# Optimization experiments

Hardware: AMD Instinct MI355X
Metric: run time of the kernel (lower is better)

Reference implementation:

```python
import jax, jax.numpy as jnp
import numpy as np

N_CONST = 1.0
M_CONST = 11008.0

def setup_inputs() -> dict:
    key = jax.random.key(0)
    ks = jax.random.split(key, 7)
    N, LM_D, GNN_D, H = 131072, 1024, 200, 128
    lm_embeds = jax.random.normal(ks[0], (N, LM_D), dtype=jnp.float32)
    gnn_embeds = jax.random.normal(ks[1], (N, GNN_D), dtype=jnp.float32)
    neg_gnn_embeds = jax.random.normal(ks[2], (N, GNN_D), dtype=jnp.float32)
    lm_W = jax.random.normal(ks[3], (LM_D, H), dtype=jnp.float32) * (1.0 / np.sqrt(LM_D))
    lm_b = jnp.zeros((H,), dtype=jnp.float32)
    gnn_W = jax.random.normal(ks[4], (GNN_D, H), dtype=jnp.float32) * (1.0 / np.sqrt(GNN_D))
    gnn_b = jnp.zeros((H,), dtype=jnp.float32)
    return {"lm_embeds": lm_embeds, "gnn_embeds": gnn_embeds,
            "neg_gnn_embeds": neg_gnn_embeds,
            "lm_W": lm_W, "lm_b": lm_b, "gnn_W": gnn_W, "gnn_b": gnn_b}

def _l2norm(x):
    return x / jnp.linalg.norm(x, axis=-1, keepdims=True)

def _cal(lm_in, gnn_in, lm_W, lm_b, gnn_W, gnn_b, neg):
    l = _l2norm(lm_in @ lm_W + lm_b)       # [N, H]
    g = _l2norm(gnn_in @ gnn_W + gnn_b)    # [N, H]
    # diagonal of l @ g.T == per-row dot product (avoids NxN matmul)
    logits = jnp.exp(jnp.sum(l * g, axis=-1))  # [N]
    ratio = logits / (logits + N_CONST / M_CONST)
    return jnp.log(1.0 - ratio) if neg else jnp.log(ratio)

def reference(lm_embeds, gnn_embeds, neg_gnn_embeds, lm_W, lm_b, gnn_W, gnn_b):
    pos = jnp.mean(_cal(lm_embeds, gnn_embeds, lm_W, lm_b, gnn_W, gnn_b, False))
    neg = jnp.mean(_cal(lm_embeds, neg_gnn_embeds, lm_W, lm_b, gnn_W, gnn_b, True))
    return -pos - neg
```

## Files before the change

kernel.cpp:

```cpp
#include <hip/hip_runtime.h>
#include <hip/hip_bf16.h>
#include <stdint.h>

#define NROWS 131072
#define LMD   1024
#define GNND  200
#define HD    128
#define BLOCK 256
#define MTILE 64
#define NBLK  (NROWS/MTILE)
#define WCH   16384

typedef __attribute__((ext_vector_type(4))) float  f32x4;
typedef __attribute__((ext_vector_type(8))) short  bf16x8;

#define GLDS(SRC, DST) __builtin_amdgcn_global_load_lds( \
    (const __attribute__((address_space(1))) unsigned int*)(SRC), \
    (__attribute__((address_space(3))) unsigned int*)(DST), 16, 0, 0)
#define SCHED0  __builtin_amdgcn_sched_barrier(0)
#define BAR     __builtin_amdgcn_s_barrier()
#define VMW(N)  asm volatile("s_waitcnt vmcnt(" #N ")" ::: "memory")

__device__ __forceinline__ short f2bf(float x) {
    union { __hip_bfloat16 h; short s; } u;
    u.h = __float2bfloat16(x);
    return u.s;
}

__device__ __forceinline__ bf16x8 cvt8(f32x4 a, f32x4 b) {
    bf16x8 r;
    r[0]=f2bf(a[0]); r[1]=f2bf(a[1]); r[2]=f2bf(a[2]); r[3]=f2bf(a[3]);
    r[4]=f2bf(b[0]); r[5]=f2bf(b[1]); r[6]=f2bf(b[2]); r[7]=f2bf(b[3]);
    return r;
}

__device__ __forceinline__ float red16(float v) {
    #pragma unroll
    for (int m=1; m<16; m<<=1) v += __shfl_xor(v, m, 16);
    return v;
}

__global__ void prep_weights(const float* __restrict__ lm_W,
                             const float* __restrict__ gnn_W,
                             short* __restrict__ W1S, short* __restrict__ W2S)
{
    int idx = blockIdx.x*BLOCK + threadIdx.x;
    int row = (idx >> 6) & 127;
    int e   = idx & 63;
    int kk  = (idx >> 13)*64 + (e ^ ((row & 7)*8));
    W1S[idx] = f2bf(lm_W[(long)kk*HD + row]);
    if (idx < 4*8192) {
        W2S[idx] = (kk < GNND) ? f2bf(gnn_W[(long)kk*HD + row]) : (short)0;
    }
}

__global__ __launch_bounds__(BLOCK) void fused(
    const float* __restrict__ lm,  const float* __restrict__ gnn,
    const float* __restrict__ ngn,
    const float* __restrict__ lm_b, const float* __restrict__ gnn_b,
    const char* __restrict__ W1S,  const char* __restrict__ W2S,
    float* __restrict__ partials)
{
    __shared__ short lbuf[4*8192];
    __shared__ float sp[4], sn[4];

    const int tid  = threadIdx.x;
    const int lane = tid & 63;
    const int win  = tid >> 6;
    const int col  = lane & 15;
    const int g    = lane >> 4;
    const int wq   = win*4096 + lane*16;
    const long row = (long)blockIdx.x * MTILE + win*16 + col;

    const char* aL = (const char*)lm  + row*(LMD*4L)  + g*32;
    const char* aG = (const char*)gnn + row*(GNND*4L) + g*32;
    const char* aN = (const char*)ngn + row*(GNND*4L) + g*32;
    const char* clampG = (const char*)gnn + (size_t)NROWS*GNND*4 - 16;
    const char* clampN = (const char*)ngn + (size_t)NROWS*GNND*4 - 16;

    const float CC   = 1.0f / 11008.0f;
    const float LOGC = -9.3063777f;
    const f32x4 fz = {0.f,0.f,0.f,0.f};

    auto ISSUEW = [&](int x) {
        const char* ws = (x < 16 ? W1S + (size_t)x*WCH : W2S + (size_t)(x-16)*WCH) + wq;
        char* wd = (char*)lbuf + (size_t)(x & 3)*WCH + wq;
        #pragma unroll
        for (int i=0;i<4;i++) GLDS(ws + i*1024, wd + i*1024);
    };
    auto LOADG = [&](const char* base, int off, const char* cl, f32x4 (&S)[8]) {
        #pragma unroll
        for (int j=0;j<4;j++) {
            const char* p0 = base + off + j*128;
            const char* p1 = p0 + 16;
            if (cl) { if (p0 > cl) p0 = cl;  if (p1 > cl) p1 = cl; }
            S[2*j]   = *(const f32x4*)p0;
            S[2*j+1] = *(const f32x4*)p1;
        }
    };
    auto COMP = [&](int c, int half, f32x4 (&S)[8], f32x4 (&acc)[8]) {
        const short* wb = lbuf + (c & 3)*8192 + col*64;
        const int sw = (col & 7)*8;
        #pragma unroll
        for (int ks=0; ks<2; ++ks) {
            bf16x8 af = cvt8(S[half*4 + 2*ks], S[half*4 + 2*ks + 1]);
            const short* cb = wb + ((ks*32 + g*8) ^ sw);
            #pragma unroll
            for (int t=0;t<8;t++) {
                bf16x8 wf = *(const bf16x8*)(cb + t*1024);
                acc[t] = __builtin_amdgcn_mfma_f32_16x16x32_bf16(af, wf, acc[t], 0,0,0);
            }
        }
    };

    f32x4 accL[8], accG[8];
    #pragma unroll
    for (int t=0;t<8;t++) accL[t] = fz;
    f32x4 SA[8], SB[8];
    float pos_acc = 0.f, neg_acc = 0.f;

    float bl[8], bg[8];
    #pragma unroll
    for (int t=0;t<8;t++) bl[t] = lm_b[t*16+col];
    #pragma unroll
    for (int t=0;t<8;t++) bg[t] = gnn_b[t*16+col];
    SCHED0;
    ISSUEW(0); ISSUEW(1); ISSUEW(2);
    LOADG(aL,   0, nullptr, SA);
    LOADG(aL, 512, nullptr, SB);
    SCHED0; VMW(24); SCHED0; BAR; SCHED0;
    #pragma unroll
    for (int t=0;t<8;t++) { asm volatile("" : "+v"(bl[t])); asm volatile("" : "+v"(bg[t])); }

    #pragma unroll
    for (int gg=0; gg<8; ++gg) {
        f32x4 (&S)[8] = (gg & 1) ? SB : SA;
        ISSUEW(2*gg+3);
        SCHED0;
        COMP(2*gg, 0, S, accL);
        SCHED0; VMW(16); SCHED0; BAR; SCHED0;
        ISSUEW(2*gg+4);
        SCHED0;
        COMP(2*gg+1, 1, S, accL);
        SCHED0;
        if (gg < 6)       LOADG(aL, (gg+2)*512, nullptr, S);
        else if (gg == 6) LOADG(aG,   0, clampG, S);
        else              LOADG(aG, 512, clampG, S);
        SCHED0; VMW(24); SCHED0; BAR; SCHED0;
    }

    #pragma unroll
    for (int t=0;t<8;t++) {
        #pragma unroll
        for (int r=0;r<4;r++) accL[t][r] += bl[t];
    }
    #pragma unroll
    for (int t=0;t<8;t++) accG[t] = fz;

    ISSUEW(19);
    SCHED0;
    COMP(16, 0, SA, accG);
    SCHED0; VMW(16); SCHED0; BAR; SCHED0;

    COMP(17, 1, SA, accG);
    SCHED0;
    LOADG(aN, 0, clampN, SA);
    SCHED0; VMW(20); SCHED0; BAR; SCHED0;

    COMP(18, 0, SB, accG);
    SCHED0; VMW(8); SCHED0; BAR; SCHED0;

    COMP(19, 1, SB, accG);
    SCHED0;
    LOADG(aN, 512, clampN, SB);
    SCHED0;

    #pragma unroll
    for (int r=0;r<4;r++) {
        float lg=0.f, ll=0.f, gg2=0.f;
        #pragma unroll
        for (int t=0;t<8;t++) {
            float lv=accL[t][r], gv=accG[t][r]+bg[t];
            lg += lv*gv; ll += lv*lv; gg2 += gv*gv;
        }
        lg=red16(lg); ll=red16(ll); gg2=red16(gg2);
        float d  = lg * rsqrtf(ll*gg2);
        float pi = d - logf(expf(d)+CC);
        if (col==0) pos_acc += pi;
    }
    #pragma unroll
    for (int t=0;t<8;t++) accG[t] = fz;

    COMP(20, 0, SA, accG);
    COMP(21, 1, SA, accG);
    COMP(22, 0, SB, accG);
    COMP(23, 1, SB, accG);

    #pragma unroll
    for (int r=0;r<4;r++) {
        float ln=0.f, nn=0.f, ll=0.f;
        #pragma unroll
        for (int t=0;t<8;t++) {
            float lv=accL[t][r], nv=accG[t][r]+bg[t];
            ln += lv*nv; nn += nv*nv; ll += lv*lv;
        }
        ln=red16(ln); nn=red16(nn); ll=red16(ll);
        float d  = ln * rsqrtf(ll*nn);
        float ni = LOGC - logf(expf(d)+CC);
        if (col==0) neg_acc += ni;
    }

    #pragma unroll
    for (int m=1;m<64;m<<=1) {
        pos_acc += __shfl_xor(pos_acc, m, 64);
        neg_acc += __shfl_xor(neg_acc, m, 64);
    }
    if (lane==0) { sp[win]=pos_acc; sn[win]=neg_acc; }
    __syncthreads();
    if (tid==0) {
        float p=0.f,n=0.f;
        #pragma unroll
        for (int w=0;w<4;w++){ p+=sp[w]; n+=sn[w]; }
        partials[blockIdx.x*2]   = p;
        partials[blockIdx.x*2+1] = n;
    }
}

__global__ void finalize(const float* __restrict__ partials, float* __restrict__ out)
{
    __shared__ float sp[BLOCK], sn[BLOCK];
    float p=0.f, n=0.f;
    for (int i=threadIdx.x; i<NBLK; i+=BLOCK) { p += partials[2*i]; n += partials[2*i+1]; }
    sp[threadIdx.x]=p; sn[threadIdx.x]=n;
    __syncthreads();
    for (int s=BLOCK/2; s>0; s>>=1) {
        if (threadIdx.x < s) { sp[threadIdx.x]+=sp[threadIdx.x+s]; sn[threadIdx.x]+=sn[threadIdx.x+s]; }
        __syncthreads();
    }
    if (threadIdx.x==0) out[0] = -(sp[0]+sn[0]) / (float)NROWS;
}

extern "C" void kernel_launch(void* const* d_in, const int* in_sizes, int n_in,
                              void* d_out, int out_size, void* d_ws, size_t ws_size,
                              hipStream_t stream)
{
    const float* lm    = (const float*)d_in[0];
    const float* gnn   = (const float*)d_in[1];
    const float* ngn   = (const float*)d_in[2];
    const float* lm_W  = (const float*)d_in[3];
    const float* lm_b  = (const float*)d_in[4];
    const float* gnn_W = (const float*)d_in[5];
    const float* gnn_b = (const float*)d_in[6];

    short* W1S = (short*)d_ws;
    short* W2S = (short*)((char*)d_ws + 262144);
    float* partials = (float*)((char*)d_ws + 262144 + 65536);

    prep_weights<<<512, BLOCK, 0, stream>>>(lm_W, gnn_W, W1S, W2S);
    fused<<<NBLK, BLOCK, 0, stream>>>(lm, gnn, ngn, lm_b, gnn_b,
                                      (const char*)W1S, (const char*)W2S, partials);
    finalize<<<1, BLOCK, 0, stream>>>(partials, (float*)d_out);
}
```

Measured before the change: 180.3 us.

## Cut LDS to three weight buffers for 3 blocks/CU, fuse finalize via atomic counter

New measurement: 312.5 us. +73.3%, slower.

```diff
diff --git a/kernel.cpp b/kernel.cpp
--- a/kernel.cpp
+++ b/kernel.cpp
@@ -42,9 +42,11 @@
 
 __global__ void prep_weights(const float* __restrict__ lm_W,
                              const float* __restrict__ gnn_W,
-                             short* __restrict__ W1S, short* __restrict__ W2S)
+                             short* __restrict__ W1S, short* __restrict__ W2S,
+                             unsigned int* counter)
 {
     int idx = blockIdx.x*BLOCK + threadIdx.x;
+    if (idx == 0) *counter = 0;
     int row = (idx >> 6) & 127;
     int e   = idx & 63;
     int kk  = (idx >> 13)*64 + (e ^ ((row & 7)*8));
@@ -54,15 +56,17 @@
     }
 }
 
-__global__ __launch_bounds__(BLOCK) void fused(
+__global__ __launch_bounds__(BLOCK, 3) void fused(
     const float* __restrict__ lm,  const float* __restrict__ gnn,
     const float* __restrict__ ngn,
     const float* __restrict__ lm_b, const float* __restrict__ gnn_b,
     const char* __restrict__ W1S,  const char* __restrict__ W2S,
-    float* __restrict__ partials)
+    float* partials, unsigned int* counter, float* out)
 {
-    __shared__ short lbuf[4*8192];
+    __shared__ short lbuf[3*8192];
+    __shared__ float bias_lds[256];
     __shared__ float sp[4], sn[4];
+    __shared__ int   lastflag;
 
     const int tid  = threadIdx.x;
     const int lane = tid & 63;
@@ -82,11 +86,18 @@
     const float LOGC = -9.3063777f;
     const f32x4 fz = {0.f,0.f,0.f,0.f};
 
-    auto ISSUEW = [&](int x) {
-        const char* ws = (x < 16 ? W1S + (size_t)x*WCH : W2S + (size_t)(x-16)*WCH) + wq;
-        char* wd = (char*)lbuf + (size_t)(x & 3)*WCH + wq;
-        #pragma unroll
-        for (int i=0;i<4;i++) GLDS(ws + i*1024, wd + i*1024);
+    if (tid < 64) {
+        f32x4 bv = (tid < 32) ? *(const f32x4*)((const char*)lm_b  + tid*16)
+                              : *(const f32x4*)((const char*)gnn_b + (tid-32)*16);
+        *(f32x4*)&bias_lds[tid*4] = bv;
+    }
+    SCHED0;
+
+    auto ISSUEW = [&](const char* ws, int b) {
+        const char* s = ws + wq;
+        char* d = (char*)lbuf + (size_t)b*WCH + wq;
+        #pragma unroll
+        for (int i=0;i<4;i++) GLDS(s + i*1024, d + i*1024);
     };
     auto LOADG = [&](const char* base, int off, const char* cl, f32x4 (&S)[8]) {
         #pragma unroll
@@ -98,9 +109,17 @@
             S[2*j+1] = *(const f32x4*)p1;
         }
     };
-    auto COMP = [&](int c, int half, f32x4 (&S)[8], f32x4 (&acc)[8]) {
-        const short* wb = lbuf + (c & 3)*8192 + col*64;
+
+    f32x4 SA[8], SB[8];
+    f32x4 accL[8], accG[8];
+    #pragma unroll
+    for (int t=0;t<8;t++) { accL[t] = fz; accG[t] = fz; }
+
+    auto COMP = [&](int c, f32x4 (&acc)[8]) {
+        const short* wb = lbuf + (c % 3)*8192 + col*64;
         const int sw = (col & 7)*8;
+        f32x4 (&S)[8] = ((c>>1)&1) ? SB : SA;
+        const int half = c & 1;
         #pragma unroll
         for (int ks=0; ks<2; ++ks) {
             bf16x8 af = cvt8(S[half*4 + 2*ks], S[half*4 + 2*ks + 1]);
@@ -113,68 +132,46 @@
         }
     };
 
-    f32x4 accL[8], accG[8];
-    #pragma unroll
-    for (int t=0;t<8;t++) accL[t] = fz;
-    f32x4 SA[8], SB[8];
     float pos_acc = 0.f, neg_acc = 0.f;
 
-    float bl[8], bg[8];
-    #pragma unroll
-    for (int t=0;t<8;t++) bl[t] = lm_b[t*16+col];
-    #pragma unroll
-    for (int t=0;t<8;t++) bg[t] = gnn_b[t*16+col];
-    SCHED0;
-    ISSUEW(0); ISSUEW(1); ISSUEW(2);
+    ISSUEW(W1S + 0*WCH, 0);
+    ISSUEW(W1S + 1*WCH, 1);
     LOADG(aL,   0, nullptr, SA);
     LOADG(aL, 512, nullptr, SB);
-    SCHED0; VMW(24); SCHED0; BAR; SCHED0;
-    #pragma unroll
-    for (int t=0;t<8;t++) { asm volatile("" : "+v"(bl[t])); asm volatile("" : "+v"(bg[t])); }
-
-    #pragma unroll
-    for (int gg=0; gg<8; ++gg) {
-        f32x4 (&S)[8] = (gg & 1) ? SB : SA;
-        ISSUEW(2*gg+3);
-        SCHED0;
-        COMP(2*gg, 0, S, accL);
-        SCHED0; VMW(16); SCHED0; BAR; SCHED0;
-        ISSUEW(2*gg+4);
-        SCHED0;
-        COMP(2*gg+1, 1, S, accL);
-        SCHED0;
-        if (gg < 6)       LOADG(aL, (gg+2)*512, nullptr, S);
-        else if (gg == 6) LOADG(aG,   0, clampG, S);
-        else              LOADG(aG, 512, clampG, S);
-        SCHED0; VMW(24); SCHED0; BAR; SCHED0;
-    }
-
+    SCHED0; VMW(20); SCHED0; BAR; SCHED0;
+
+    #pragma unroll
+    for (int c = 0; c < 20; ++c) {
+        {
+            const char* ws = (c <= 13) ? W1S + (size_t)(c+2)*WCH
+                           : (c <= 17) ? W2S + (size_t)(c-14)*WCH
+                                       : W2S + (size_t)(c-18)*WCH;
+            ISSUEW(ws, (c+2) % 3);
+        }
+        SCHED0;
+        if (c < 16) COMP(c, accL); else COMP(c, accG);
+        SCHED0;
+        if (c==1)  LOADG(aL, 2*512, nullptr, SA);
+        if (c==5)  LOADG(aL, 4*512, nullptr, SA);
+        if (c==9)  LOADG(aL, 6*512, nullptr, SA);
+        if (c==13) LOADG(aG,     0, clampG,  SA);
+        if (c==17) LOADG(aN,     0, clampN,  SA);
+        if (c==3)  LOADG(aL, 3*512, nullptr, SB);
+        if (c==7)  LOADG(aL, 5*512, nullptr, SB);
+        if (c==11) LOADG(aL, 7*512, nullptr, SB);
+        if (c==15) LOADG(aG,   512, clampG,  SB);
+        if (c==19) LOADG(aN,   512, clampN,  SB);
+        SCHED0; VMW(12); SCHED0; BAR; SCHED0;
+    }
+
+    float bl[8], bg[8];
+    #pragma unroll
+    for (int t=0;t<8;t++) { bl[t] = bias_lds[t*16+col]; bg[t] = bias_lds[128+t*16+col]; }
     #pragma unroll
     for (int t=0;t<8;t++) {
         #pragma unroll
         for (int r=0;r<4;r++) accL[t][r] += bl[t];
     }
-    #pragma unroll
-    for (int t=0;t<8;t++) accG[t] = fz;
-
-    ISSUEW(19);
-    SCHED0;
-    COMP(16, 0, SA, accG);
-    SCHED0; VMW(16); SCHED0; BAR; SCHED0;
-
-    COMP(17, 1, SA, accG);
-    SCHED0;
-    LOADG(aN, 0, clampN, SA);
-    SCHED0; VMW(20); SCHED0; BAR; SCHED0;
-
-    COMP(18, 0, SB, accG);
-    SCHED0; VMW(8); SCHED0; BAR; SCHED0;
-
-    COMP(19, 1, SB, accG);
-    SCHED0;
-    LOADG(aN, 512, clampN, SB);
-    SCHED0;
-
     #pragma unroll
     for (int r=0;r<4;r++) {
         float lg=0.f, ll=0.f, gg2=0.f;
@@ -191,10 +188,16 @@
     #pragma unroll
     for (int t=0;t<8;t++) accG[t] = fz;
 
-    COMP(20, 0, SA, accG);
-    COMP(21, 1, SA, accG);
-    COMP(22, 0, SB, accG);
-    COMP(23, 1, SB, accG);
+    #pragma unroll
+    for (int c = 20; c < 24; ++c) {
+        if (c <= 21) { ISSUEW(W2S + (size_t)(c-18)*WCH, (c+2) % 3); }
+        SCHED0;
+        COMP(c, accG);
+        SCHED0;
+        if (c==20)      { VMW(12); SCHED0; BAR; SCHED0; }
+        else if (c==21) { VMW(4);  SCHED0; BAR; SCHED0; }
+        else if (c==22) { VMW(0);  SCHED0; BAR; SCHED0; }
+    }
 
     #pragma unroll
     for (int r=0;r<4;r++) {
@@ -223,21 +226,28 @@
         for (int w=0;w<4;w++){ p+=sp[w]; n+=sn[w]; }
         partials[blockIdx.x*2]   = p;
         partials[blockIdx.x*2+1] = n;
-    }
-}
-
-__global__ void finalize(const float* __restrict__ partials, float* __restrict__ out)
-{
-    __shared__ float sp[BLOCK], sn[BLOCK];
-    float p=0.f, n=0.f;
-    for (int i=threadIdx.x; i<NBLK; i+=BLOCK) { p += partials[2*i]; n += partials[2*i+1]; }
-    sp[threadIdx.x]=p; sn[threadIdx.x]=n;
+        __threadfence();
+        unsigned int old = atomicAdd(counter, 1u);
+        lastflag = (old == NBLK - 1) ? 1 : 0;
+    }
     __syncthreads();
-    for (int s=BLOCK/2; s>0; s>>=1) {
-        if (threadIdx.x < s) { sp[threadIdx.x]+=sp[threadIdx.x+s]; sn[threadIdx.x]+=sn[threadIdx.x+s]; }
+
+    if (lastflag) {
+        __threadfence();
+        float p = 0.f, n = 0.f;
+        for (int i = tid; i < NBLK; i += BLOCK) {
+            p += partials[2*i];
+            n += partials[2*i+1];
+        }
+        float* red = (float*)lbuf;
+        red[tid] = p; red[BLOCK + tid] = n;
         __syncthreads();
-    }
-    if (threadIdx.x==0) out[0] = -(sp[0]+sn[0]) / (float)NROWS;
+        for (int s = BLOCK/2; s > 0; s >>= 1) {
+            if (tid < s) { red[tid] += red[tid+s]; red[BLOCK+tid] += red[BLOCK+tid+s]; }
+            __syncthreads();
+        }
+        if (tid == 0) out[0] = -(red[0] + red[BLOCK]) / (float)NROWS;
+    }
 }
 
 extern "C" void kernel_launch(void* const* d_in, const int* in_sizes, int n_in,
@@ -255,9 +265,10 @@
     short* W1S = (short*)d_ws;
     short* W2S = (short*)((char*)d_ws + 262144);
     float* partials = (float*)((char*)d_ws + 262144 + 65536);
-
-    prep_weights<<<512, BLOCK, 0, stream>>>(lm_W, gnn_W, W1S, W2S);
+    unsigned int* counter = (unsigned int*)((char*)d_ws + 262144 + 65536 + 16384);
+
+    prep_weights<<<512, BLOCK, 0, stream>>>(lm_W, gnn_W, W1S, W2S, counter);
     fused<<<NBLK, BLOCK, 0, stream>>>(lm, gnn, ngn, lm_b, gnn_b,
-                                      (const char*)W1S, (const char*)W2S, partials);
-    finalize<<<1, BLOCK, 0, stream>>>(partials, (float*)d_out);
-}
+                                      (const char*)W1S, (const char*)W2S,
+                                      partials, counter, (float*)d_out);
+}
```

## Make fused kernel persistent with LDS-staged activations and triple-buffered pipeline

Applied to the files above, without the earlier changes.

Result: slower. 214.1 us (+18.7%).

```diff
diff --git a/kernel.cpp b/kernel.cpp
--- a/kernel.cpp
+++ b/kernel.cpp
@@ -6,10 +6,14 @@
 #define LMD   1024
 #define GNND  200
 #define HD    128
-#define BLOCK 256
-#define MTILE 64
-#define NBLK  (NROWS/MTILE)
+#define BLOCK 512
+#define GRID  256
+#define NTILE 4
+#define MTILE 128
+#define ACH   32768
 #define WCH   16384
+#define LDS_W0 (3*ACH)
+#define LDS_TOT (3*ACH + 2*WCH)
 
 typedef __attribute__((ext_vector_type(4))) float  f32x4;
 typedef __attribute__((ext_vector_type(8))) short  bf16x8;
@@ -44,7 +48,7 @@
                              const float* __restrict__ gnn_W,
                              short* __restrict__ W1S, short* __restrict__ W2S)
 {
-    int idx = blockIdx.x*BLOCK + threadIdx.x;
+    int idx = blockIdx.x*256 + threadIdx.x;
     int row = (idx >> 6) & 127;
     int e   = idx & 63;
     int kk  = (idx >> 13)*64 + (e ^ ((row & 7)*8));
@@ -54,27 +58,28 @@
     }
 }
 
-__global__ __launch_bounds__(BLOCK) void fused(
+__global__ __launch_bounds__(BLOCK, 2) void fused(
     const float* __restrict__ lm,  const float* __restrict__ gnn,
     const float* __restrict__ ngn,
     const float* __restrict__ lm_b, const float* __restrict__ gnn_b,
     const char* __restrict__ W1S,  const char* __restrict__ W2S,
     float* __restrict__ partials)
 {
-    __shared__ short lbuf[4*8192];
-    __shared__ float sp[4], sn[4];
+    extern __shared__ char lbuf[];
 
     const int tid  = threadIdx.x;
     const int lane = tid & 63;
     const int win  = tid >> 6;
     const int col  = lane & 15;
     const int g    = lane >> 4;
-    const int wq   = win*4096 + lane*16;
-    const long row = (long)blockIdx.x * MTILE + win*16 + col;
-
-    const char* aL = (const char*)lm  + row*(LMD*4L)  + g*32;
-    const char* aG = (const char*)gnn + row*(GNND*4L) + g*32;
-    const char* aN = (const char*)ngn + row*(GNND*4L) + g*32;
+
+    const long R0  = (long)blockIdx.x * MTILE;
+    const long TSL = (long)GRID*MTILE*(LMD*4L);
+    const long TSG = (long)GRID*MTILE*(GNND*4L);
+
+    const char* aLb = (const char*)lm  + R0*(LMD*4L);
+    const char* aGb = (const char*)gnn + R0*(GNND*4L);
+    const char* aNb = (const char*)ngn + R0*(GNND*4L);
     const char* clampG = (const char*)gnn + (size_t)NROWS*GNND*4 - 16;
     const char* clampN = (const char*)ngn + (size_t)NROWS*GNND*4 - 16;
 
@@ -82,28 +87,57 @@
     const float LOGC = -9.3063777f;
     const f32x4 fz = {0.f,0.f,0.f,0.f};
 
-    auto ISSUEW = [&](int x) {
-        const char* ws = (x < 16 ? W1S + (size_t)x*WCH : W2S + (size_t)(x-16)*WCH) + wq;
-        char* wd = (char*)lbuf + (size_t)(x & 3)*WCH + wq;
-        #pragma unroll
-        for (int i=0;i<4;i++) GLDS(ws + i*1024, wd + i*1024);
+    float bl[8], bg[8];
+    #pragma unroll
+    for (int t=0;t<8;t++) bl[t] = lm_b[t*16+col];
+    #pragma unroll
+    for (int t=0;t<8;t++) bg[t] = gnn_b[t*16+col];
+    SCHED0;
+
+    auto STAGEW = [&](int x) {
+        const char* ws = (x < 16) ? W1S + (size_t)x*WCH
+                       : (x < 20) ? W2S + (size_t)(x-16)*WCH
+                       : (x < 24) ? W2S + (size_t)(x-20)*WCH
+                                  : W1S;
+        char* wd = lbuf + LDS_W0 + (size_t)(x & 1)*WCH;
+        #pragma unroll
+        for (int i=0;i<2;i++) {
+            int u = i*BLOCK + tid;
+            GLDS(ws + u*16, wd + u*16);
+        }
     };
-    auto LOADG = [&](const char* base, int off, const char* cl, f32x4 (&S)[8]) {
-        #pragma unroll
-        for (int j=0;j<4;j++) {
-            const char* p0 = base + off + j*128;
-            const char* p1 = p0 + 16;
-            if (cl) { if (p0 > cl) p0 = cl;  if (p1 > cl) p1 = cl; }
-            S[2*j]   = *(const f32x4*)p0;
-            S[2*j+1] = *(const f32x4*)p1;
+
+    auto STAGEA = [&](int x) {
+        const char* base; long rowB; const char* cl;
+        if (x >= 24)     { base = aLb + TSL + (size_t)(x-24)*256; rowB = LMD*4L;  cl = nullptr; }
+        else if (x < 16) { base = aLb + (size_t)x*256;            rowB = LMD*4L;  cl = nullptr; }
+        else if (x < 20) { base = aGb + (size_t)(x-16)*256;       rowB = GNND*4L; cl = clampG; }
+        else             { base = aNb + (size_t)(x-20)*256;       rowB = GNND*4L; cl = clampN; }
+        char* ad = lbuf + (size_t)(x % 3)*ACH;
+        #pragma unroll
+        for (int i=0;i<4;i++) {
+            int u  = i*BLOCK + tid;
+            int r  = u >> 4;
+            int sg = (u & 15) ^ (r & 7);
+            const char* src = base + (long)r*rowB + sg*16;
+            if (cl && src > cl) src = cl;
+            GLDS(src, ad + u*16);
         }
     };
-    auto COMP = [&](int c, int half, f32x4 (&S)[8], f32x4 (&acc)[8]) {
-        const short* wb = lbuf + (c & 3)*8192 + col*64;
-        const int sw = (col & 7)*8;
+
+    const int rb = (win*16 + col) * 256;
+    const int s7 = col & 7;
+    const int sw = (col & 7) * 8;
+
+    auto COMP = [&](int c, f32x4 (&acc)[8]) {
+        const char*  ab = lbuf + (size_t)(c % 3)*ACH;
+        const short* wb = (const short*)(lbuf + LDS_W0 + (size_t)(c & 1)*WCH) + col*64;
         #pragma unroll
         for (int ks=0; ks<2; ++ks) {
-            bf16x8 af = cvt8(S[half*4 + 2*ks], S[half*4 + 2*ks + 1]);
+            const int u0 = ks*8 + g*2;
+            f32x4 a0 = *(const f32x4*)(ab + rb + (((u0    ) ^ s7) << 4));
+            f32x4 a1 = *(const f32x4*)(ab + rb + (((u0 + 1) ^ s7) << 4));
+            bf16x8 af = cvt8(a0, a1);
             const short* cb = wb + ((ks*32 + g*8) ^ sw);
             #pragma unroll
             for (int t=0;t<8;t++) {
@@ -113,101 +147,86 @@
         }
     };
 
-    f32x4 accL[8], accG[8];
-    #pragma unroll
-    for (int t=0;t<8;t++) accL[t] = fz;
-    f32x4 SA[8], SB[8];
     float pos_acc = 0.f, neg_acc = 0.f;
 
-    float bl[8], bg[8];
-    #pragma unroll
-    for (int t=0;t<8;t++) bl[t] = lm_b[t*16+col];
-    #pragma unroll
-    for (int t=0;t<8;t++) bg[t] = gnn_b[t*16+col];
-    SCHED0;
-    ISSUEW(0); ISSUEW(1); ISSUEW(2);
-    LOADG(aL,   0, nullptr, SA);
-    LOADG(aL, 512, nullptr, SB);
-    SCHED0; VMW(24); SCHED0; BAR; SCHED0;
+    STAGEW(0); STAGEA(0); STAGEW(1); STAGEA(1);
+    SCHED0; VMW(6); SCHED0; BAR; SCHED0;
     #pragma unroll
     for (int t=0;t<8;t++) { asm volatile("" : "+v"(bl[t])); asm volatile("" : "+v"(bg[t])); }
 
-    #pragma unroll
-    for (int gg=0; gg<8; ++gg) {
-        f32x4 (&S)[8] = (gg & 1) ? SB : SA;
-        ISSUEW(2*gg+3);
-        SCHED0;
-        COMP(2*gg, 0, S, accL);
-        SCHED0; VMW(16); SCHED0; BAR; SCHED0;
-        ISSUEW(2*gg+4);
-        SCHED0;
-        COMP(2*gg+1, 1, S, accL);
-        SCHED0;
-        if (gg < 6)       LOADG(aL, (gg+2)*512, nullptr, S);
-        else if (gg == 6) LOADG(aG,   0, clampG, S);
-        else              LOADG(aG, 512, clampG, S);
-        SCHED0; VMW(24); SCHED0; BAR; SCHED0;
-    }
-
-    #pragma unroll
-    for (int t=0;t<8;t++) {
-        #pragma unroll
-        for (int r=0;r<4;r++) accL[t][r] += bl[t];
-    }
-    #pragma unroll
-    for (int t=0;t<8;t++) accG[t] = fz;
-
-    ISSUEW(19);
-    SCHED0;
-    COMP(16, 0, SA, accG);
-    SCHED0; VMW(16); SCHED0; BAR; SCHED0;
-
-    COMP(17, 1, SA, accG);
-    SCHED0;
-    LOADG(aN, 0, clampN, SA);
-    SCHED0; VMW(20); SCHED0; BAR; SCHED0;
-
-    COMP(18, 0, SB, accG);
-    SCHED0; VMW(8); SCHED0; BAR; SCHED0;
-
-    COMP(19, 1, SB, accG);
-    SCHED0;
-    LOADG(aN, 512, clampN, SB);
-    SCHED0;
-
-    #pragma unroll
-    for (int r=0;r<4;r++) {
-        float lg=0.f, ll=0.f, gg2=0.f;
+    #pragma unroll 1
+    for (int t4 = 0; t4 < NTILE; ++t4) {
+        const bool lastT = (t4 == NTILE-1);
+        f32x4 accL[8], accG[8];
+        #pragma unroll
+        for (int t=0;t<8;t++) accL[t] = fz;
+
+        #pragma unroll
+        for (int c = 0; c < 16; ++c) {
+            if (c > 0 || t4 > 0) STAGEW(c+1);
+            STAGEA(c+2);
+            SCHED0;
+            COMP(c, accL);
+            SCHED0; VMW(4); SCHED0; BAR; SCHED0;
+        }
         #pragma unroll
         for (int t=0;t<8;t++) {
-            float lv=accL[t][r], gv=accG[t][r]+bg[t];
-            lg += lv*gv; ll += lv*lv; gg2 += gv*gv;
-        }
-        lg=red16(lg); ll=red16(ll); gg2=red16(gg2);
-        float d  = lg * rsqrtf(ll*gg2);
-        float pi = d - logf(expf(d)+CC);
-        if (col==0) pos_acc += pi;
-    }
-    #pragma unroll
-    for (int t=0;t<8;t++) accG[t] = fz;
-
-    COMP(20, 0, SA, accG);
-    COMP(21, 1, SA, accG);
-    COMP(22, 0, SB, accG);
-    COMP(23, 1, SB, accG);
-
-    #pragma unroll
-    for (int r=0;r<4;r++) {
-        float ln=0.f, nn=0.f, ll=0.f;
-        #pragma unroll
-        for (int t=0;t<8;t++) {
-            float lv=accL[t][r], nv=accG[t][r]+bg[t];
-            ln += lv*nv; nn += nv*nv; ll += lv*lv;
-        }
-        ln=red16(ln); nn=red16(nn); ll=red16(ll);
-        float d  = ln * rsqrtf(ll*nn);
-        float ni = LOGC - logf(expf(d)+CC);
-        if (col==0) neg_acc += ni;
+            #pragma unroll
+            for (int r=0;r<4;r++) accL[t][r] += bl[t];
+        }
+        #pragma unroll
+        for (int t=0;t<8;t++) accG[t] = fz;
+
+        #pragma unroll
+        for (int c = 16; c < 20; ++c) {
+            STAGEW(c+1);
+            STAGEA(c+2);
+            SCHED0;
+            COMP(c, accG);
+            SCHED0; VMW(4); SCHED0; BAR; SCHED0;
+        }
+        #pragma unroll
+        for (int r=0;r<4;r++) {
+            float lg=0.f, ll=0.f, gg2=0.f;
+            #pragma unroll
+            for (int t=0;t<8;t++) {
+                float lv=accL[t][r], gv=accG[t][r]+bg[t];
+                lg += lv*gv; ll += lv*lv; gg2 += gv*gv;
+            }
+            lg=red16(lg); ll=red16(ll); gg2=red16(gg2);
+            float d  = lg * rsqrtf(ll*gg2);
+            float pi = d - logf(expf(d)+CC);
+            if (col==0) pos_acc += pi;
+        }
+        #pragma unroll
+        for (int t=0;t<8;t++) accG[t] = fz;
+
+        #pragma unroll
+        for (int c = 20; c < 24; ++c) {
+            if (c < 23 || !lastT) STAGEW(c+1);
+            if (c < 22 || !lastT) STAGEA(c+2);
+            SCHED0;
+            COMP(c, accG);
+            SCHED0;
+            if (!lastT)          { VMW(4); SCHED0; BAR; SCHED0; }
+            else if (c < 22)     { VMW(4); SCHED0; BAR; SCHED0; }
+            else if (c == 22)    { VMW(0); SCHED0; BAR; SCHED0; }
+        }
+        #pragma unroll
+        for (int r=0;r<4;r++) {
+            float ln=0.f, nn=0.f, ll=0.f;
+            #pragma unroll
+            for (int t=0;t<8;t++) {
+                float lv=accL[t][r], nv=accG[t][r]+bg[t];
+                ln += lv*nv; nn += nv*nv; ll += lv*lv;
+            }
+            ln=red16(ln); nn=red16(nn); ll=red16(ll);
+            float d  = ln * rsqrtf(ll*nn);
+            float ni = LOGC - logf(expf(d)+CC);
+            if (col==0) neg_acc += ni;
+        }
+
+        aLb += TSL; aGb += TSG; aNb += TSG;
     }
 
     #pragma unroll
@@ -215,12 +234,15 @@
         pos_acc += __shfl_xor(pos_acc, m, 64);
         neg_acc += __shfl_xor(neg_acc, m, 64);
     }
+    __syncthreads();
+    float* sp = (float*)lbuf;
+    float* sn = sp + 8;
     if (lane==0) { sp[win]=pos_acc; sn[win]=neg_acc; }
     __syncthreads();
     if (tid==0) {
         float p=0.f,n=0.f;
         #pragma unroll
-        for (int w=0;w<4;w++){ p+=sp[w]; n+=sn[w]; }
+        for (int w=0;w<8;w++){ p+=sp[w]; n+=sn[w]; }
         partials[blockIdx.x*2]   = p;
         partials[blockIdx.x*2+1] = n;
     }
@@ -228,13 +250,13 @@
 
 __global__ void finalize(const float* __restrict__ partials, float* __restrict__ out)
 {
-    __shared__ float sp[BLOCK], sn[BLOCK];
+    __shared__ float sp[256], sn[256];
     float p=0.f, n=0.f;
-    for (int i=threadIdx.x; i<NBLK; i+=BLOCK) { p += partials[2*i]; n += partials[2*i+1]; }
+    for (int i=threadIdx.x; i<GRID; i+=256) { p += partials[2*i]; n += partials[2*i+1]; }
     sp[threadIdx.x]=p; sn[threadIdx.x]=n;
     __syncthreads();
-    for (int s=BLOCK/2; s>0; s>>=1) {
-        if (threadIdx.x < s) { sp[threadIdx.x]+=sp[threadIdx.x+s]; sn[threadIdx.x]+=sn[threadIdx.x+s]; }
+    for (int s=128; s>0; s>>=1) {
+        if ((int)threadIdx.x < s) { sp[threadIdx.x]+=sp[threadIdx.x+s]; sn[threadIdx.x]+=sn[threadIdx.x+s]; }
         __syncthreads();
     }
     if (threadIdx.x==0) out[0] = -(sp[0]+sn[0]) / (float)NROWS;
@@ -256,8 +278,11 @@
     short* W2S = (short*)((char*)d_ws + 262144);
     float* partials = (float*)((char*)d_ws + 262144 + 65536);
 
-    prep_weights<<<512, BLOCK, 0, stream>>>(lm_W, gnn_W, W1S, W2S);
-    fused<<<NBLK, BLOCK, 0, stream>>>(lm, gnn, ngn, lm_b, gnn_b,
-                                      (const char*)W1S, (const char*)W2S, partials);
-    finalize<<<1, BLOCK, 0, stream>>>(partials, (float*)d_out);
-}
+    hipFuncSetAttribute((const void*)fused,
+                        hipFuncAttributeMaxDynamicSharedMemorySize, LDS_TOT);
+
+    prep_weights<<<512, 256, 0, stream>>>(lm_W, gnn_W, W1S, W2S);
+    fused<<<GRID, BLOCK, LDS_TOT, stream>>>(lm, gnn, ngn, lm_b, gnn_b,
+                                            (const char*)W1S, (const char*)W2S, partials);
+    finalize<<<1, 256, 0, stream>>>(partials, (float*)d_out);
+}
```
